# Optimization experiments

Measured on AMD Instinct MI355X. Metric: run time of the kernel, lower is better.

## Reference

```python
import jax, jax.numpy as jnp
import numpy as np


def setup_inputs() -> dict:
    N, E, F_IN, H, C = 100000, 3200000, 128, 16, 2
    key = jax.random.key(0)
    k1, k2, k3, k4 = jax.random.split(key, 4)
    x = jax.random.normal(k1, (N, F_IN), dtype=jnp.float32)
    edge_index = jax.random.randint(k2, (2, E), 0, N, dtype=jnp.int64)
    W1 = jax.random.normal(k3, (F_IN, H), dtype=jnp.float32) * (1.0 / np.sqrt(F_IN))
    b1 = jnp.zeros((H,), dtype=jnp.float32)
    W2 = jax.random.normal(k4, (H, C), dtype=jnp.float32) * (1.0 / np.sqrt(H))
    b2 = jnp.zeros((C,), dtype=jnp.float32)
    return {"x": x, "edge_index": edge_index, "W1": W1, "b1": b1, "W2": W2, "b2": b2}


def _gcn_norm(edge_index, num_nodes):
    # PyG gcn_norm: add self-loops, deg from destination, norm = d^-1/2[src]*d^-1/2[dst]
    loop = jnp.arange(num_nodes, dtype=edge_index.dtype)
    src = jnp.concatenate([edge_index[0], loop])
    dst = jnp.concatenate([edge_index[1], loop])
    deg = jax.ops.segment_sum(jnp.ones_like(src, dtype=jnp.float32), dst,
                              num_segments=num_nodes)
    dinv = jnp.where(deg > 0, jax.lax.rsqrt(deg), 0.0)
    norm = dinv[src] * dinv[dst]  # [E + N]
    return src, dst, norm


def _gcn_conv(h, src, dst, norm, W, b, num_nodes):
    h = h @ W                       # dense transform first (in >= out channels)
    msg = h[src] * norm[:, None]    # gather + normalize, [E+N, out]
    agg = jax.ops.segment_sum(msg, dst, num_segments=num_nodes)
    return agg + b


def reference(x, edge_index, W1, b1, W2, b2):
    N = x.shape[0]
    src, dst, norm = _gcn_norm(edge_index, N)
    h = jax.nn.relu(_gcn_conv(x, src, dst, norm, W1, b1, N))
    out = _gcn_conv(h, src, dst, norm, W2, b2, N)
    return out
```

## Files before the change

kernel.cpp:

```cpp
#include <hip/hip_runtime.h>


#define EPB  8192
#define RCAP 12288
#define CAP  16384

typedef unsigned int u32;
typedef unsigned short u16;

__device__ __forceinline__ float bflo(u32 u) { return __uint_as_float(u << 16); }
__device__ __forceinline__ float bfhi(u32 u) { return __uint_as_float(u & 0xffff0000u); }
__device__ __forceinline__ u32 pack_bf2(float a, float b) {
    u32 ua = __float_as_uint(a); ua = (ua + 0x7fffu + ((ua >> 16) & 1u)) >> 16;
    u32 ub = __float_as_uint(b); ub = (ub + 0x7fffu + ((ub >> 16) & 1u)) >> 16;
    return ua | (ub << 16);
}

__global__ __launch_bounds__(512) void k_binit(int* __restrict__ gcur, int NBUK) {
    int t = threadIdx.x;
    if (t < NBUK) gcur[t] = t * RCAP;
}

__global__ __launch_bounds__(512) void k_fat(const int* __restrict__ ei,
                                             int* __restrict__ gcur,
                                             u32* __restrict__ part,
                                             const float* __restrict__ x,
                                             const float* __restrict__ W1,
                                             float* __restrict__ hraw,
                                             int E, int NBUK, int NSCAT, int N) {
    __shared__ union {
        struct { int hist[512]; int rbase[512]; u32 buf[EPB]; u16 bkt[EPB]; } s;
        float w[4 * 516];
    } sm;
    int tid = threadIdx.x;
    if ((int)blockIdx.x < NSCAT) {
        sm.s.hist[tid] = 0;
        __syncthreads();
        int base = blockIdx.x * EPB;
        int end = base + EPB; if (end > E) end = E;
        int cnt = end - base;
        int nv = cnt >> 2;
        const int4* s4p = (const int4*)(ei + base);
        const int4* d4p = (const int4*)(ei + E + base);
        int4 s4[4], d4[4];
        #pragma unroll
        for (int k = 0; k < 4; ++k) {
            int idx = tid + (k << 9);
            if (idx < nv) {
                s4[k] = s4p[idx];
                d4[k] = d4p[idx];
                atomicAdd(&sm.s.hist[d4[k].x >> 8], 1);
                atomicAdd(&sm.s.hist[d4[k].y >> 8], 1);
                atomicAdd(&sm.s.hist[d4[k].z >> 8], 1);
                atomicAdd(&sm.s.hist[d4[k].w >> 8], 1);
            }
        }
        for (int e = base + (nv << 2) + tid; e < end; e += 512)
            atomicAdd(&sm.s.hist[ei[E + e] >> 8], 1);
        __syncthreads();
        int v = sm.s.hist[tid];
        __syncthreads();
        for (int o = 1; o < 512; o <<= 1) {
            int t = (tid >= o) ? sm.s.hist[tid - o] : 0;
            __syncthreads();
            sm.s.hist[tid] += t;
            __syncthreads();
        }
        int excl = sm.s.hist[tid] - v;
        int rb = 0;
        if (tid < NBUK && v > 0) rb = atomicAdd(&gcur[tid], v);
        sm.s.rbase[tid] = rb - excl;
        __syncthreads();
        sm.s.hist[tid] = excl;
        __syncthreads();
        #pragma unroll
        for (int k = 0; k < 4; ++k) {
            int idx = tid + (k << 9);
            if (idx < nv) {
                int b, pos;
                b = d4[k].x >> 8; pos = atomicAdd(&sm.s.hist[b], 1);
                sm.s.buf[pos] = ((u32)(d4[k].x & 255) << 24) | (u32)s4[k].x; sm.s.bkt[pos] = (u16)b;
                b = d4[k].y >> 8; pos = atomicAdd(&sm.s.hist[b], 1);
                sm.s.buf[pos] = ((u32)(d4[k].y & 255) << 24) | (u32)s4[k].y; sm.s.bkt[pos] = (u16)b;
                b = d4[k].z >> 8; pos = atomicAdd(&sm.s.hist[b], 1);
                sm.s.buf[pos] = ((u32)(d4[k].z & 255) << 24) | (u32)s4[k].z; sm.s.bkt[pos] = (u16)b;
                b = d4[k].w >> 8; pos = atomicAdd(&sm.s.hist[b], 1);
                sm.s.buf[pos] = ((u32)(d4[k].w & 255) << 24) | (u32)s4[k].w; sm.s.bkt[pos] = (u16)b;
            }
        }
        for (int e = base + (nv << 2) + tid; e < end; e += 512) {
            int s = ei[e], d = ei[E + e];
            int b = d >> 8;
            int pos = atomicAdd(&sm.s.hist[b], 1);
            sm.s.buf[pos] = ((u32)(d & 255) << 24) | (u32)s;
            sm.s.bkt[pos] = (u16)b;
        }
        __syncthreads();
        for (int j = tid; j < cnt; j += 512)
            part[sm.s.rbase[sm.s.bkt[j]] + j] = sm.s.buf[j];
    } else {
        for (int t = tid; t < 2048; t += 512)
            sm.w[(t >> 9) * 516 + (t & 511)] = W1[t];
        __syncthreads();
        int t = ((int)blockIdx.x - NSCAT) * 512 + tid;
        int n = t >> 2, q = t & 3;
        if (n >= N) return;
        const float4* xr = (const float4*)(x + (size_t)n * 128 + q * 32);
        const float* ws = sm.w + q * 516;
        float acc[16];
        #pragma unroll
        for (int c = 0; c < 16; ++c) acc[c] = 0.f;
        #pragma unroll
        for (int i = 0; i < 8; ++i) {
            float4 u = xr[i];
            const float4* wf = (const float4*)(ws + i * 64);
            #pragma unroll
            for (int c4 = 0; c4 < 4; ++c4) {
                float4 wa = wf[c4];
                float4 wb = wf[4 + c4];
                float4 wc = wf[8 + c4];
                float4 wd = wf[12 + c4];
                int c = c4 * 4;
                acc[c+0] = fmaf(u.x, wa.x, acc[c+0]); acc[c+1] = fmaf(u.x, wa.y, acc[c+1]);
                acc[c+2] = fmaf(u.x, wa.z, acc[c+2]); acc[c+3] = fmaf(u.x, wa.w, acc[c+3]);
                acc[c+0] = fmaf(u.y, wb.x, acc[c+0]); acc[c+1] = fmaf(u.y, wb.y, acc[c+1]);
                acc[c+2] = fmaf(u.y, wb.z, acc[c+2]); acc[c+3] = fmaf(u.y, wb.w, acc[c+3]);
                acc[c+0] = fmaf(u.z, wc.x, acc[c+0]); acc[c+1] = fmaf(u.z, wc.y, acc[c+1]);
                acc[c+2] = fmaf(u.z, wc.z, acc[c+2]); acc[c+3] = fmaf(u.z, wc.w, acc[c+3]);
                acc[c+0] = fmaf(u.w, wd.x, acc[c+0]); acc[c+1] = fmaf(u.w, wd.y, acc[c+1]);
                acc[c+2] = fmaf(u.w, wd.z, acc[c+2]); acc[c+3] = fmaf(u.w, wd.w, acc[c+3]);
            }
        }
        #pragma unroll
        for (int c = 0; c < 16; ++c) {
            acc[c] += __shfl_xor(acc[c], 1);
            acc[c] += __shfl_xor(acc[c], 2);
        }
        ((float4*)(hraw + (size_t)n * 16))[q] =
            make_float4(acc[4*q+0], acc[4*q+1], acc[4*q+2], acc[4*q+3]);
    }
}

__global__ __launch_bounds__(512) void k_fillB(const u32* __restrict__ part,
                                               const int* __restrict__ gcur,
                                               u32* __restrict__ csr,
                                               int* __restrict__ rp,
                                               float* __restrict__ dinv,
                                               const float* __restrict__ hraw,
                                               u16* __restrict__ hs,
                                               int N, int E, int NBUK) {
    __shared__ int hist[256];
    __shared__ int ofs[256];
    __shared__ int bs[512];
    __shared__ u32 srcbuf[CAP];
    int b = blockIdx.x, tid = threadIdx.x;
    if (b == 0 && tid == 0) rp[N] = E;
    int vb = (tid < NBUK) ? (gcur[tid] - tid * RCAP) : 0;
    bs[tid] = vb;
    if (tid < 256) hist[tid] = 0;
    __syncthreads();
    for (int o = 1; o < 512; o <<= 1) {
        int t = (tid >= o) ? bs[tid - o] : 0;
        __syncthreads();
        bs[tid] += t;
        __syncthreads();
    }
    int cnt = gcur[b] - b * RCAP;
    int base_w = bs[b] - cnt;
    int base_r = b * RCAP;
    int nv = cnt >> 2;
    const uint4* p4 = (const uint4*)(part + base_r);
    for (int t = tid; t < nv; t += 512) {
        uint4 pv = p4[t];
        atomicAdd(&hist[pv.x >> 24], 1);
        atomicAdd(&hist[pv.y >> 24], 1);
        atomicAdd(&hist[pv.z >> 24], 1);
        atomicAdd(&hist[pv.w >> 24], 1);
    }
    for (int j = (nv << 2) + tid; j < cnt; j += 512)
        atomicAdd(&hist[part[base_r + j] >> 24], 1);
    __syncthreads();
    int v = 0;
    if (tid < 256) { v = hist[tid]; ofs[tid] = v; }
    __syncthreads();
    for (int o = 1; o < 256; o <<= 1) {
        int t = 0;
        if (tid < 256 && tid >= o) t = ofs[tid - o];
        __syncthreads();
        if (tid < 256) ofs[tid] += t;
        __syncthreads();
    }
    int excl = 0;
    if (tid < 256) { excl = ofs[tid] - v; hist[tid] = excl; }
    __syncthreads();
    for (int t = tid; t < nv; t += 512) {
        uint4 pv = p4[t];
        int pos;
        pos = atomicAdd(&hist[pv.x >> 24], 1);
        if (pos < CAP) srcbuf[pos] = pv.x & 0xFFFFFFu;
        pos = atomicAdd(&hist[pv.y >> 24], 1);
        if (pos < CAP) srcbuf[pos] = pv.y & 0xFFFFFFu;
        pos = atomicAdd(&hist[pv.z >> 24], 1);
        if (pos < CAP) srcbuf[pos] = pv.z & 0xFFFFFFu;
        pos = atomicAdd(&hist[pv.w >> 24], 1);
        if (pos < CAP) srcbuf[pos] = pv.w & 0xFFFFFFu;
    }
    for (int j = (nv << 2) + tid; j < cnt; j += 512) {
        u32 pv = part[base_r + j];
        int pos = atomicAdd(&hist[pv >> 24], 1);
        if (pos < CAP) srcbuf[pos] = pv & 0xFFFFFFu;
    }
    __syncthreads();
    for (int j = tid; j < cnt; j += 512)
        csr[base_w + j] = srcbuf[j];
    int d = b * 256 + tid;
    if (tid < 256 && d < N) {
        rp[d] = base_w + excl;
        float dval = rsqrtf((float)(v + 1));
        dinv[d] = dval;
        ((float*)ofs)[tid] = dval;
    }
    __syncthreads();
    int dn = b * 256 + (tid >> 1);
    if (dn < N) {
        float di = ((float*)ofs)[tid >> 1];
        int h = tid & 1;
        const float4* hr = (const float4*)(hraw + (size_t)dn * 16);
        float4 A = hr[h * 2], B = hr[h * 2 + 1];
        uint4 o;
        o.x = pack_bf2(A.x * di, A.y * di);
        o.y = pack_bf2(A.z * di, A.w * di);
        o.z = pack_bf2(B.x * di, B.y * di);
        o.w = pack_bf2(B.z * di, B.w * di);
        ((uint4*)(hs + (size_t)dn * 16))[h] = o;
    }
}

__global__ __launch_bounds__(256) void k_agg1h2(const int* __restrict__ rp,
                                                const int* __restrict__ csr,
                                                const u16* __restrict__ hs,
                                                const float* __restrict__ dinv,
                                                const float* __restrict__ W2,
                                                const float* __restrict__ b1,
                                                float* __restrict__ h2s, int N) {
    int lane = threadIdx.x & 63;
    int wid = blockIdx.x * 16 + (threadIdx.x >> 6) * 4 + (lane >> 4);
    if (wid >= N) return;
    int l = lane & 15;
    int half = l & 1, g = l >> 1;
    int beg = rp[wid], end = rp[wid + 1];
    float a0 = 0.f, a1 = 0.f, a2 = 0.f, a3 = 0.f;
    float a4 = 0.f, a5 = 0.f, a6 = 0.f, a7 = 0.f;
    for (int j = beg + g; j < end; j += 8) {
        int s = csr[j];
        uint4 u = ((const uint4*)(hs + (size_t)s * 16))[half];
        a0 += bflo(u.x); a1 += bfhi(u.x);
        a2 += bflo(u.y); a3 += bfhi(u.y);
        a4 += bflo(u.z); a5 += bfhi(u.z);
        a6 += bflo(u.w); a7 += bfhi(u.w);
    }
    a0 += __shfl_xor(a0, 2); a1 += __shfl_xor(a1, 2);
    a2 += __shfl_xor(a2, 2); a3 += __shfl_xor(a3, 2);
    a4 += __shfl_xor(a4, 2); a5 += __shfl_xor(a5, 2);
    a6 += __shfl_xor(a6, 2); a7 += __shfl_xor(a7, 2);
    a0 += __shfl_xor(a0, 4); a1 += __shfl_xor(a1, 4);
    a2 += __shfl_xor(a2, 4); a3 += __shfl_xor(a3, 4);
    a4 += __shfl_xor(a4, 4); a5 += __shfl_xor(a5, 4);
    a6 += __shfl_xor(a6, 4); a7 += __shfl_xor(a7, 4);
    a0 += __shfl_xor(a0, 8); a1 += __shfl_xor(a1, 8);
    a2 += __shfl_xor(a2, 8); a3 += __shfl_xor(a3, 8);
    a4 += __shfl_xor(a4, 8); a5 += __shfl_xor(a5, 8);
    a6 += __shfl_xor(a6, 8); a7 += __shfl_xor(a7, 8);
    uint4 su = ((const uint4*)(hs + (size_t)wid * 16))[half];
    a0 += bflo(su.x); a1 += bfhi(su.x);
    a2 += bflo(su.y); a3 += bfhi(su.y);
    a4 += bflo(su.z); a5 += bfhi(su.z);
    a6 += bflo(su.w); a7 += bfhi(su.w);
    float di = dinv[wid];
    float4 bA = ((const float4*)b1)[half * 2];
    float4 bB = ((const float4*)b1)[half * 2 + 1];
    float v0 = fmaxf(fmaf(di, a0, bA.x), 0.f);
    float v1 = fmaxf(fmaf(di, a1, bA.y), 0.f);
    float v2 = fmaxf(fmaf(di, a2, bA.z), 0.f);
    float v3 = fmaxf(fmaf(di, a3, bA.w), 0.f);
    float v4 = fmaxf(fmaf(di, a4, bB.x), 0.f);
    float v5 = fmaxf(fmaf(di, a5, bB.y), 0.f);
    float v6 = fmaxf(fmaf(di, a6, bB.z), 0.f);
    float v7 = fmaxf(fmaf(di, a7, bB.w), 0.f);
    const float4* w4 = (const float4*)W2 + half * 4;
    float4 q0 = w4[0], q1 = w4[1], q2 = w4[2], q3 = w4[3];
    float p0 = v0*q0.x + v1*q0.z + v2*q1.x + v3*q1.z
             + v4*q2.x + v5*q2.z + v6*q3.x + v7*q3.z;
    float p1 = v0*q0.y + v1*q0.w + v2*q1.y + v3*q1.w
             + v4*q2.y + v5*q2.w + v6*q3.y + v7*q3.w;
    p0 += __shfl_xor(p0, 1); p1 += __shfl_xor(p1, 1);
    if (l == 0)
        *(float2*)(h2s + (size_t)wid * 2) = make_float2(p0 * di, p1 * di);
}

__global__ __launch_bounds__(256) void k_agg2(const int* __restrict__ rp,
                                              const int* __restrict__ csr,
                                              const float* __restrict__ h2s,
                                              const float* __restrict__ dinv,
                                              const float* __restrict__ b2,
                                              float* __restrict__ out, int N) {
    int lane = threadIdx.x & 63;
    int wid = blockIdx.x * 16 + (threadIdx.x >> 6) * 4 + (lane >> 4);
    if (wid >= N) return;
    int l = lane & 15;
    int beg = rp[wid], end = rp[wid + 1];
    float a0 = 0.f, a1 = 0.f;
    for (int j = beg + l; j < end; j += 16) {
        int s = csr[j];
        float2 v = *(const float2*)(h2s + (size_t)s * 2);
        a0 += v.x; a1 += v.y;
    }
    a0 += __shfl_xor(a0, 1); a1 += __shfl_xor(a1, 1);
    a0 += __shfl_xor(a0, 2); a1 += __shfl_xor(a1, 2);
    a0 += __shfl_xor(a0, 4); a1 += __shfl_xor(a1, 4);
    a0 += __shfl_xor(a0, 8); a1 += __shfl_xor(a1, 8);
    if (l == 0) {
        float di = dinv[wid];
        float2 sv = *(const float2*)(h2s + (size_t)wid * 2);
        *(float2*)(out + (size_t)wid * 2) =
            make_float2(fmaf(di, a0 + sv.x, b2[0]), fmaf(di, a1 + sv.y, b2[1]));
    }
}

extern "C" void kernel_launch(void* const* d_in, const int* in_sizes, int n_in,
                              void* d_out, int out_size, void* d_ws, size_t ws_size,
                              hipStream_t stream) {
    const float* x  = (const float*)d_in[0];
    const int*   ei = (const int*)d_in[1];
    const float* W1 = (const float*)d_in[2];
    const float* b1 = (const float*)d_in[3];
    const float* W2 = (const float*)d_in[4];
    const float* b2 = (const float*)d_in[5];
    float* out = (float*)d_out;

    const int N = in_sizes[0] / 128;
    const int E = in_sizes[1] / 2;
    const int NBUK = (N + 255) / 256;
    const int NPB  = (E + EPB - 1) / EPB;
    const int NXW  = (N * 4 + 511) / 512;

    char* ws = (char*)d_ws;
    size_t off = 0;
    auto alloc = [&](size_t bytes) {
        void* p = ws + off;
        off = (off + bytes + 255) & ~(size_t)255;
        return p;
    };
    u32*   part  = (u32*)alloc((size_t)NBUK * RCAP * 4);
    u32*   csr   = (u32*)alloc((size_t)E * 4);
    int*   rp    = (int*)alloc((size_t)(N + 1) * 4);
    float* dinv  = (float*)alloc((size_t)N * 4);
    float* hraw  = (float*)alloc((size_t)N * 16 * 4);
    u16*   hs    = (u16*)alloc((size_t)N * 16 * 2);
    float* h2s   = (float*)alloc((size_t)N * 2 * 4);
    int*   gcur  = (int*)alloc((size_t)NBUK * 4);

    k_binit  <<<dim3(1),          dim3(512), 0, stream>>>(gcur, NBUK);
    k_fat    <<<dim3(NPB + NXW),  dim3(512), 0, stream>>>(ei, gcur, part, x, W1, hraw, E, NBUK, NPB, N);
    k_fillB  <<<dim3(NBUK),       dim3(512), 0, stream>>>(part, gcur, csr, rp, dinv, hraw, hs, N, E, NBUK);
    k_agg1h2 <<<dim3((N + 15) / 16), dim3(256), 0, stream>>>(rp, (const int*)csr, hs, dinv, W2, b1, h2s, N);
    k_agg2   <<<dim3((N + 15) / 16), dim3(256), 0, stream>>>(rp, (const int*)csr, h2s, dinv, b2, out, N);
}
```

Baseline: 179.2 us.

## Sort nodes by degree within buckets for balanced aggregation; shrink scatter chunk

In the fill kernel, each 256-node bucket is counting-sorted by in-degree (capped at 127) into a permutation array. Both aggregation kernels then process nodes in that order, so the 16-lane groups sharing a wavefront get similar edge counts and less divergence. Separately, edges per scatter block drop from 8192 to 6144, which adds blocks and changes register and shared-memory use. The cost is an extra indirection load per node, scattered writes to the outputs, and a sort step at the end of the fill kernel.

Result: slower. 201.9 us (+12.7%).

```diff
diff --git a/kernel.cpp b/kernel.cpp
--- a/kernel.cpp
+++ b/kernel.cpp
@@ -1,7 +1,7 @@
 #include <hip/hip_runtime.h>
 
 
-#define EPB  8192
+#define EPB  6144
 #define RCAP 12288
 #define CAP  16384
 
@@ -42,9 +42,9 @@
         int nv = cnt >> 2;
         const int4* s4p = (const int4*)(ei + base);
         const int4* d4p = (const int4*)(ei + E + base);
-        int4 s4[4], d4[4];
-        #pragma unroll
-        for (int k = 0; k < 4; ++k) {
+        int4 s4[3], d4[3];
+        #pragma unroll
+        for (int k = 0; k < 3; ++k) {
             int idx = tid + (k << 9);
             if (idx < nv) {
                 s4[k] = s4p[idx];
@@ -74,7 +74,7 @@
         sm.s.hist[tid] = excl;
         __syncthreads();
         #pragma unroll
-        for (int k = 0; k < 4; ++k) {
+        for (int k = 0; k < 3; ++k) {
             int idx = tid + (k << 9);
             if (idx < nv) {
                 int b, pos;
@@ -148,6 +148,7 @@
                                                float* __restrict__ dinv,
                                                const float* __restrict__ hraw,
                                                u16* __restrict__ hs,
+                                               int* __restrict__ perm,
                                                int N, int E, int NBUK) {
     __shared__ int hist[256];
     __shared__ int ofs[256];
@@ -234,6 +235,25 @@
         o.w = pack_bf2(B.z * di, B.w * di);
         ((uint4*)(hs + (size_t)dn * 16))[h] = o;
     }
+    __syncthreads();
+    if (tid < 256) bs[tid] = 0;
+    __syncthreads();
+    bool valid = (tid < 256) && (d < N);
+    int dg = 0;
+    if (valid) { dg = v > 127 ? 127 : v; atomicAdd(&bs[dg], 1); }
+    __syncthreads();
+    for (int o = 1; o < 128; o <<= 1) {
+        int t = 0;
+        if (tid < 128 && tid >= o) t = bs[tid - o];
+        __syncthreads();
+        if (tid < 128) bs[tid] += t;
+        __syncthreads();
+    }
+    if (valid) {
+        int rank0 = dg ? bs[dg - 1] : 0;
+        int r = atomicAdd(&bs[128 + dg], 1);
+        perm[b * 256 + rank0 + r] = d;
+    }
 }
 
 __global__ __launch_bounds__(256) void k_agg1h2(const int* __restrict__ rp,
@@ -242,10 +262,12 @@
                                                 const float* __restrict__ dinv,
                                                 const float* __restrict__ W2,
                                                 const float* __restrict__ b1,
+                                                const int* __restrict__ perm,
                                                 float* __restrict__ h2s, int N) {
     int lane = threadIdx.x & 63;
-    int wid = blockIdx.x * 16 + (threadIdx.x >> 6) * 4 + (lane >> 4);
-    if (wid >= N) return;
+    int wid0 = blockIdx.x * 16 + (threadIdx.x >> 6) * 4 + (lane >> 4);
+    if (wid0 >= N) return;
+    int wid = perm[wid0];
     int l = lane & 15;
     int half = l & 1, g = l >> 1;
     int beg = rp[wid], end = rp[wid + 1];
@@ -303,10 +325,12 @@
                                               const float* __restrict__ h2s,
                                               const float* __restrict__ dinv,
                                               const float* __restrict__ b2,
+                                              const int* __restrict__ perm,
                                               float* __restrict__ out, int N) {
     int lane = threadIdx.x & 63;
-    int wid = blockIdx.x * 16 + (threadIdx.x >> 6) * 4 + (lane >> 4);
-    if (wid >= N) return;
+    int wid0 = blockIdx.x * 16 + (threadIdx.x >> 6) * 4 + (lane >> 4);
+    if (wid0 >= N) return;
+    int wid = perm[wid0];
     int l = lane & 15;
     int beg = rp[wid], end = rp[wid + 1];
     float a0 = 0.f, a1 = 0.f;
@@ -358,11 +382,12 @@
     float* hraw  = (float*)alloc((size_t)N * 16 * 4);
     u16*   hs    = (u16*)alloc((size_t)N * 16 * 2);
     float* h2s   = (float*)alloc((size_t)N * 2 * 4);
+    int*   perm  = (int*)alloc((size_t)N * 4);
     int*   gcur  = (int*)alloc((size_t)NBUK * 4);
 
     k_binit  <<<dim3(1),          dim3(512), 0, stream>>>(gcur, NBUK);
     k_fat    <<<dim3(NPB + NXW),  dim3(512), 0, stream>>>(ei, gcur, part, x, W1, hraw, E, NBUK, NPB, N);
-    k_fillB  <<<dim3(NBUK),       dim3(512), 0, stream>>>(part, gcur, csr, rp, dinv, hraw, hs, N, E, NBUK);
-    k_agg1h2 <<<dim3((N + 15) / 16), dim3(256), 0, stream>>>(rp, (const int*)csr, hs, dinv, W2, b1, h2s, N);
-    k_agg2   <<<dim3((N + 15) / 16), dim3(256), 0, stream>>>(rp, (const int*)csr, h2s, dinv, b2, out, N);
-}
+    k_fillB  <<<dim3(NBUK),       dim3(512), 0, stream>>>(part, gcur, csr, rp, dinv, hraw, hs, perm, N, E, NBUK);
+    k_agg1h2 <<<dim3((N + 15) / 16), dim3(256), 0, stream>>>(rp, (const int*)csr, hs, dinv, W2, b1, perm, h2s, N);
+    k_agg2   <<<dim3((N + 15) / 16), dim3(256), 0, stream>>>(rp, (const int*)csr, h2s, dinv, b2, perm, out, N);
+}
```
